# Optimization experiments

Measured on AMD Instinct MI355X. Metric: run time of the kernel, lower is better.

Reference implementation:

```python
import jax, jax.numpy as jnp
import numpy as np

H = 128      # hidden_channels
C = 5        # input_channels
B = 2048     # batch
G = 10       # grid size


def _conv(x, w, b, pad):
    # x: [B,Cin,H,W], w: [Cout,Cin,kh,kw]
    y = jax.lax.conv_general_dilated(
        x, w, window_strides=(1, 1), padding=[(pad, pad), (pad, pad)],
        dimension_numbers=('NCHW', 'OIHW', 'NCHW'))
    return y + b[None, :, None, None]


def setup_inputs() -> dict:
    key = jax.random.key(0)
    ks = jax.random.split(key, 16)
    s = 0.05  # weight init scale
    inp = {
        'x': jax.random.uniform(ks[0], (B, C, G, G), dtype=jnp.float32),
        'w_p1': jax.random.normal(ks[1], (H, C, 3, 3), jnp.float32) * s,
        'b_p1': jnp.zeros((H,), jnp.float32),
        'w_p2': jax.random.normal(ks[2], (H, H, 3, 3), jnp.float32) * s,
        'b_p2': jnp.zeros((H,), jnp.float32),
        'w_p3': jax.random.normal(ks[3], (H, H, 1, 1), jnp.float32) * s,
        'b_p3': jnp.zeros((H,), jnp.float32),
        'w_u1': jax.random.normal(ks[4], (H, H, 1, 1), jnp.float32) * s,
        'b_u1': jnp.zeros((H,), jnp.float32),
        'w_u2': jax.random.normal(ks[5], (H, H, 1, 1), jnp.float32) * s,
        'b_u2': jnp.zeros((H,), jnp.float32),
        'w_u3': jax.random.normal(ks[6], (H, H, 1, 1), jnp.float32) * s,
        'b_u3': jnp.zeros((H,), jnp.float32),
        'w_u4': jax.random.normal(ks[7], (C, H, 1, 1), jnp.float32) * s,
        'b_u4': jnp.zeros((C,), jnp.float32),
        'steps': 50,
    }
    return inp


def reference(x, w_p1, b_p1, w_p2, b_p2, w_p3, b_p3,
              w_u1, b_u1, w_u2, b_u2, w_u3, b_u3, w_u4, b_u4, steps):
    relu = jax.nn.relu
    steps_f = jnp.float32(steps)

    def step_fn(x, step):
        dx = relu(_conv(x, w_p1, b_p1, 1))
        dx = relu(_conv(dx, w_p2, b_p2, 1))
        dx = relu(_conv(dx, w_p3, b_p3, 0))
        dx = relu(_conv(dx, w_u1, b_u1, 0))
        dx = relu(_conv(dx, w_u2, b_u2, 0))
        dx = relu(_conv(dx, w_u3, b_u3, 0))
        dx = _conv(dx, w_u4, b_u4, 0)
        x = x + dx
        temperature = jnp.maximum(1.0 - step / steps_f, 0.5)
        x = jax.nn.softmax(x / temperature, axis=1)
        return x, x

    x_final, states = jax.lax.scan(step_fn, x, jnp.arange(steps, dtype=jnp.float32))
    # states: [steps, B, C, G, G] — stacked analogue of the python list
    return x_final, states
```

## Files before the change

kernel.cpp:

```cpp
#include <hip/hip_runtime.h>
#include <cstdint>
#include <cstddef>


#define NSAMPLES 2048
#define ZROW_BASE 28672
#define HA_OFF 0
#define HB_OFF 28928
#define A1_OFF HB_OFF
#define XS_OFF 57600
#define LDS_TOTAL 62976

typedef __attribute__((ext_vector_type(8))) short bf16x8;
typedef __attribute__((ext_vector_type(4))) float f32x4;
typedef __attribute__((ext_vector_type(2))) unsigned int u32x2;
typedef __attribute__((ext_vector_type(4))) unsigned int u32x4;

#define MFMA16(A,B,C) __builtin_amdgcn_mfma_f32_16x16x32_bf16((A),(B),(C),0,0,0)

__device__ __forceinline__ unsigned pk2(float a, float b) {
  unsigned r;
  asm("v_cvt_pk_bf16_f32 %0, %1, %2" : "=v"(r) : "v"(a), "v"(b));
  return r;
}
__device__ __forceinline__ unsigned pk2r(float a, float b) {
  return pk2(fmaxf(a, 0.f), fmaxf(b, 0.f));
}

__device__ __forceinline__ short f2bf(float f) {
  unsigned u = __float_as_uint(f);
  return (short)((u + 0x7FFFu + ((u >> 16) & 1u)) >> 16);
}

__global__ void prepack_kernel(const float* __restrict__ w, short* __restrict__ dst,
                               int mode, int ntc, int Kact, int Nact, int total) {
  int idx = blockIdx.x * 256 + threadIdx.x;
  if (idx >= total) return;
  int j = idx & 7, l = (idx >> 3) & 63, t = idx >> 9;
  int nt = t % ntc, kt = t / ntc;
  int kg = kt * 32 + (l >> 4) * 8 + j;
  int nn = nt * 16 + (l & 15);
  float v = 0.f;
  if (mode == 0) {
    if (kg < Kact && nn < Nact) v = w[nn * Kact + kg];
  } else if (mode == 1) {
    if (kg < 45) { int s = kg / 5, cin = kg - 5 * s; v = w[nn * 45 + cin * 9 + s]; }
  } else {
    int s = kt >> 2;
    int kk = (kt & 3) * 32 + (l >> 4) * 8 + j;
    v = w[nn * 1152 + kk * 9 + s];
  }
  dst[idx] = f2bf(v);
}

__device__ __forceinline__ void load_w4(bf16x8 (&W)[2][4], const short* __restrict__ p,
                                        int w, int l) {
#pragma unroll
  for (int mt = 0; mt < 2; ++mt)
#pragma unroll
    for (int kt = 0; kt < 4; ++kt)
      W[mt][kt] = *(const bf16x8*)&p[((kt * 8 + 2 * w + mt) * 64 + l) * 8];
}
__device__ __forceinline__ void load_b(f32x4 (&pb)[2], const float* __restrict__ bp,
                                       int w, int g) {
  pb[0] = *(const f32x4*)&bp[16 * (2 * w) + 4 * g];
  pb[1] = *(const f32x4*)&bp[16 * (2 * w + 1) + 4 * g];
}

__device__ __forceinline__ void chain_mfma(const bf16x8 (&W)[2][4], const f32x4 (&pb)[2],
                                           const char* lds, int rdb, f32x4 (&acc)[2][7]) {
#pragma unroll
  for (int qt = 0; qt < 7; ++qt) { acc[0][qt] = pb[0]; acc[1][qt] = pb[1]; }
#pragma unroll
  for (int kt = 0; kt < 4; ++kt) {
    const char* src = lds + (rdb ^ (kt << 6));
#pragma unroll
    for (int qt = 0; qt < 7; ++qt) {
      bf16x8 Bf = *(const bf16x8*)(src + qt * 4096);
      acc[0][qt] = MFMA16(W[0][kt], Bf, acc[0][qt]);
      acc[1][qt] = MFMA16(W[1][kt], Bf, acc[1][qt]);
    }
  }
}

__device__ __forceinline__ void store_h(const f32x4 (&acc)[2][7], char* lds,
                                        int wb0, int wb1) {
#pragma unroll
  for (int mt = 0; mt < 2; ++mt) {
    char* d = lds + (mt ? wb1 : wb0);
#pragma unroll
    for (int qt = 0; qt < 7; ++qt) {
      f32x4 v = acc[mt][qt];
      u32x2 wv = {pk2r(v.x, v.y), pk2r(v.z, v.w)};
      *(u32x2*)(d + qt * 4096) = wv;
    }
  }
}

__global__ __launch_bounds__(256, 2)
void nca_kernel(
    const float* __restrict__ x_in,
    const float* __restrict__ b1p, const float* __restrict__ b2p,
    const float* __restrict__ b3p, const float* __restrict__ b4p,
    const float* __restrict__ b5p, const float* __restrict__ b6p,
    const float* __restrict__ b7p,
    const short* __restrict__ W1, const short* __restrict__ W2,
    const short* __restrict__ W3,
    const short* __restrict__ W7,
    const int* __restrict__ steps_ptr, float* __restrict__ d_out) {
  __shared__ __align__(16) char lds[LDS_TOTAL];
  float* xs = (float*)(lds + XS_OFF);

  const int tid = threadIdx.x;
  const int sample = blockIdx.x;
  const int w = tid >> 6;
  const int l = tid & 63;
  const int n = l & 15;
  const int g = l >> 4;
  const int g16 = g << 4;
  const int swzc = (n & 7) << 4;
  const int steps = *steps_ptr;
  const float steps_f = (float)steps;
  const f32x4 fz = {0.f, 0.f, 0.f, 0.f};

  const int rdA = HA_OFF + n * 256 + (g16 ^ swzc);
  const int rdB = HB_OFF + n * 256 + (g16 ^ swzc);
  const int rd1 = A1_OFF + n * 128 + (g16 ^ swzc);
  const int wcol0 = ((64 * w) | (8 * g)) ^ swzc;
  const int wcol1 = ((64 * w + 32) | (8 * g)) ^ swzc;
  const int wbA0 = HA_OFF + n * 256 + wcol0, wbA1 = HA_OFF + n * 256 + wcol1;
  const int wbB0 = HB_OFF + n * 256 + wcol0, wbB1 = HB_OFF + n * 256 + wcol1;
  int zadj[7];
#pragma unroll
  for (int qt = 0; qt < 7; ++qt) zadj[qt] = HA_OFF + ZROW_BASE + g16 - 4096 * qt;

  int rc[7];
#pragma unroll
  for (int qt = 0; qt < 7; ++qt) {
    int p = 16 * qt + n;
    if (p < 100) { int r = p / 10; rc[qt] = r * 32 + (p - 10 * r); }
    else rc[qt] = 0x4000;
  }
  const int cA = tid / 100, pA = tid - 100 * cA;
  const int cB = (tid + 256) / 100, pB = tid + 256 - 100 * cB;
  const int offA = pA * 12 + cA, offB = pB * 12 + cB;

  if (tid < 64) *(unsigned*)(lds + HA_OFF + ZROW_BASE + tid * 4) = 0;
  xs[offA] = x_in[(size_t)sample * 500 + tid];
  if (tid < 244) xs[offB] = x_in[(size_t)sample * 500 + tid + 256];
  f32x4 b7v = fz;
  if (g == 0) b7v = *(const f32x4*)&b7p[0];
  else if (g == 1) b7v.x = b7p[4];
  __syncthreads();

  for (int step = 0; step < steps; ++step) {
    if (step > 0) {
      size_t sb = 1024000u + ((size_t)(step - 1) * NSAMPLES + sample) * 500u;
      __builtin_nontemporal_store(xs[offA], &d_out[sb + tid]);
      if (tid < 244) __builtin_nontemporal_store(xs[offB], &d_out[sb + tid + 256]);
    }
    if (tid < 112) {
      const int p = tid;
      const bool pv = p < 100;
      const int pc = pv ? p : 99;
      const int r = pc / 10, c0 = pc - 10 * r;
      float val[48];
#pragma unroll
      for (int s = 0; s < 9; ++s) {
        const int dr = s / 3 - 1, dc = s % 3 - 1;
        f32x4 xv = fz; float x4v = 0.f;
        if (pv && (unsigned)(r + dr) < 10u && (unsigned)(c0 + dc) < 10u) {
          const float* xr = &xs[(p + dr * 10 + dc) * 12];
          xv = *(const f32x4*)xr; x4v = xr[4];
        }
        val[5*s+0] = xv.x; val[5*s+1] = xv.y; val[5*s+2] = xv.z;
        val[5*s+3] = xv.w; val[5*s+4] = x4v;
      }
      val[45] = val[46] = val[47] = 0.f;
      unsigned wd[24];
#pragma unroll
      for (int i = 0; i < 24; ++i) wd[i] = pk2(val[2*i], val[2*i+1]);
      const int swzr = (p & 7) << 4;
      char* arow = lds + A1_OFF + p * 128;
#pragma unroll
      for (int j = 0; j < 6; ++j) {
        u32x4 wv = {wd[4*j], wd[4*j+1], wd[4*j+2], wd[4*j+3]};
        *(u32x4*)(arow + ((16 * j) ^ swzr)) = wv;
      }
      u32x4 z4 = {0, 0, 0, 0};
      *(u32x4*)(arow + (96 ^ swzr)) = z4;
      *(u32x4*)(arow + (112 ^ swzr)) = z4;
    }
    __syncthreads();

    {
      bf16x8 Wf[2][2];
#pragma unroll
      for (int mt = 0; mt < 2; ++mt)
#pragma unroll
        for (int kt = 0; kt < 2; ++kt)
          Wf[mt][kt] = *(const bf16x8*)&W1[((kt * 8 + 2 * w + mt) * 64 + l) * 8];
      f32x4 pb[2];
      load_b(pb, b1p, w, g);
      f32x4 acc[2][7];
#pragma unroll
      for (int qt = 0; qt < 7; ++qt) { acc[0][qt] = pb[0]; acc[1][qt] = pb[1]; }
#pragma unroll
      for (int kt = 0; kt < 2; ++kt) {
        const char* src = lds + (rd1 ^ (kt << 6));
#pragma unroll
        for (int qt = 0; qt < 7; ++qt) {
          bf16x8 Bf = *(const bf16x8*)(src + qt * 2048);
          acc[0][qt] = MFMA16(Wf[0][kt], Bf, acc[0][qt]);
          acc[1][qt] = MFMA16(Wf[1][kt], Bf, acc[1][qt]);
        }
      }
      store_h(acc, lds, wbA0, wbA1);
    }
    __syncthreads();

    {
      f32x4 acc[2][7];
      {
        f32x4 pb[2];
        load_b(pb, b2p, w, g);
#pragma unroll
        for (int qt = 0; qt < 7; ++qt) { acc[0][qt] = pb[0]; acc[1][qt] = pb[1]; }
      }
#pragma unroll 1
      for (int s = 0; s < 9; ++s) {
        const int s3 = s / 3;
        const int dr = s3 - 1, dc = s - 3 * s3 - 1;
        bf16x8 Wf[2][4];
        load_w4(Wf, W2 + s * 16384, w, l);
        const int ps = n + dr * 10 + dc;
        const int bs = HA_OFF + ps * 256 + (g16 ^ ((ps & 7) << 4));
#pragma unroll
        for (int qt = 0; qt < 7; ++qt) {
          bool ok = ((unsigned)((rc[qt] >> 5) + dr) < 10u) &&
                    ((unsigned)((rc[qt] & 31) + dc) < 10u);
          int va = ok ? bs : zadj[qt];
#pragma unroll
          for (int kt = 0; kt < 4; ++kt) {
            bf16x8 Bf = *(const bf16x8*)(lds + (va ^ (kt << 6)) + qt * 4096);
            acc[0][qt] = MFMA16(Wf[0][kt], Bf, acc[0][qt]);
            acc[1][qt] = MFMA16(Wf[1][kt], Bf, acc[1][qt]);
          }
        }
      }
      store_h(acc, lds, wbB0, wbB1);
    }
    __syncthreads();

#pragma unroll 1
    for (int li = 0; li < 4; ++li) {
      const float* bp = (li == 0) ? b3p : (li == 1) ? b4p : (li == 2) ? b5p : b6p;
      const int rdb = (li & 1) ? rdA : rdB;
      const int wb0 = (li & 1) ? wbB0 : wbA0;
      const int wb1 = (li & 1) ? wbB1 : wbA1;
      bf16x8 Wf[2][4];
      load_w4(Wf, W3 + li * 16384, w, l);
      f32x4 pb[2];
      load_b(pb, bp, w, g);
      f32x4 acc[2][7];
      chain_mfma(Wf, pb, lds, rdb, acc);
      store_h(acc, lds, wb0, wb1);
      __syncthreads();
    }

    {
      bf16x8 W7f[4];
#pragma unroll
      for (int kt = 0; kt < 4; ++kt)
        W7f[kt] = *(const bf16x8*)&W7[(kt * 64 + l) * 8];
      float invT = 1.f / fmaxf(1.f - (float)step / steps_f, 0.5f);
#pragma unroll
      for (int rep = 0; rep < 2; ++rep) {
        int qt = 2 * w + rep;
        if (qt < 7) {
          f32x4 a = b7v;
          int va7 = rdB + qt * 4096;
#pragma unroll
          for (int kt = 0; kt < 4; ++kt) {
            bf16x8 Bf = *(const bf16x8*)(lds + (va7 ^ (kt << 6)));
            a = MFMA16(W7f[kt], Bf, a);
          }
          float c4v = __shfl_xor(a.x, 16);
          int px = 16 * qt + n;
          if (g == 0 && px < 100) {
            float* xr = &xs[px * 12];
            f32x4 xo = *(f32x4*)xr; float x4 = xr[4];
            float v0 = (xo.x + a.x) * invT, v1 = (xo.y + a.y) * invT;
            float v2 = (xo.z + a.z) * invT, v3 = (xo.w + a.w) * invT;
            float v4 = (x4 + c4v) * invT;
            float m = fmaxf(fmaxf(fmaxf(v0, v1), fmaxf(v2, v3)), v4);
            float e0 = __expf(v0 - m), e1 = __expf(v1 - m), e2 = __expf(v2 - m);
            float e3 = __expf(v3 - m), e4 = __expf(v4 - m);
            float inv = 1.f / (e0 + e1 + e2 + e3 + e4);
            f32x4 pv = {e0 * inv, e1 * inv, e2 * inv, e3 * inv};
            *(f32x4*)xr = pv; xr[4] = e4 * inv;
          }
        }
      }
    }
    __syncthreads();
  }

  {
    size_t sb = 1024000u + ((size_t)(steps - 1) * NSAMPLES + sample) * 500u;
    size_t fb = (size_t)sample * 500u;
    float vA = xs[offA];
    __builtin_nontemporal_store(vA, &d_out[fb + tid]);
    __builtin_nontemporal_store(vA, &d_out[sb + tid]);
    if (tid < 244) {
      float vB = xs[offB];
      __builtin_nontemporal_store(vB, &d_out[fb + tid + 256]);
      __builtin_nontemporal_store(vB, &d_out[sb + tid + 256]);
    }
  }
}

extern "C" void kernel_launch(void* const* d_in, const int* in_sizes, int n_in,
                              void* d_out, int out_size, void* d_ws, size_t ws_size,
                              hipStream_t stream) {
  const float* x   = (const float*)d_in[0];
  const float* wp1 = (const float*)d_in[1];
  const float* bp1 = (const float*)d_in[2];
  const float* wp2 = (const float*)d_in[3];
  const float* bp2 = (const float*)d_in[4];
  const float* wp3 = (const float*)d_in[5];
  const float* bp3 = (const float*)d_in[6];
  const float* wu1 = (const float*)d_in[7];
  const float* bu1 = (const float*)d_in[8];
  const float* wu2 = (const float*)d_in[9];
  const float* bu2 = (const float*)d_in[10];
  const float* wu3 = (const float*)d_in[11];
  const float* bu3 = (const float*)d_in[12];
  const float* wu4 = (const float*)d_in[13];
  const float* bu4 = (const float*)d_in[14];
  const int* steps = (const int*)d_in[15];

  short* W1 = (short*)d_ws;
  short* W2 = W1 + 8192;
  short* W3 = W2 + 147456;
  short* W4 = W3 + 16384;
  short* W5 = W4 + 16384;
  short* W6 = W5 + 16384;
  short* W7 = W6 + 16384;

  prepack_kernel<<<(8192   + 255) / 256, 256, 0, stream>>>(wp1, W1, 1, 8, 45,   128, 8192);
  prepack_kernel<<<(147456 + 255) / 256, 256, 0, stream>>>(wp2, W2, 2, 8, 1152, 128, 147456);
  prepack_kernel<<<(16384  + 255) / 256, 256, 0, stream>>>(wp3, W3, 0, 8, 128,  128, 16384);
  prepack_kernel<<<(16384  + 255) / 256, 256, 0, stream>>>(wu1, W4, 0, 8, 128,  128, 16384);
  prepack_kernel<<<(16384  + 255) / 256, 256, 0, stream>>>(wu2, W5, 0, 8, 128,  128, 16384);
  prepack_kernel<<<(16384  + 255) / 256, 256, 0, stream>>>(wu3, W6, 0, 8, 128,  128, 16384);
  prepack_kernel<<<(2048   + 255) / 256, 256, 0, stream>>>(wu4, W7, 0, 1, 128,  5,   2048);

  nca_kernel<<<NSAMPLES, 256, 0, stream>>>(
      x, bp1, bp2, bp3, bu1, bu2, bu3, bu4,
      W1, W2, W3, W7, steps, (float*)d_out);
}
```

Before: 4.583 ms.

## Split MFMA work across waves by pixel tiles and drop 1x1-chain barriers

Each wave now owns two 16-pixel row tiles and computes all 128 output channels, in two 64-channel halves, instead of owning 32 channels across all seven pixel tiles. Because every wave reads and writes only its own pixel rows in the 1x1 chain, the per-layer __syncthreads there are removed. Weights are streamed from global memory per k-tile instead of being held in registers for the whole layer, and the W7 fragment load is hoisted out of the step loop. The cost is uneven load: wave 3 has only one tile while waves 0-2 have two, and weight reads through cache increase.

```diff
diff --git a/kernel.cpp b/kernel.cpp
--- a/kernel.cpp
+++ b/kernel.cpp
@@ -53,46 +53,21 @@
   dst[idx] = f2bf(v);
 }
 
-__device__ __forceinline__ void load_w4(bf16x8 (&W)[2][4], const short* __restrict__ p,
-                                        int w, int l) {
-#pragma unroll
-  for (int mt = 0; mt < 2; ++mt)
-#pragma unroll
-    for (int kt = 0; kt < 4; ++kt)
-      W[mt][kt] = *(const bf16x8*)&p[((kt * 8 + 2 * w + mt) * 64 + l) * 8];
-}
-__device__ __forceinline__ void load_b(f32x4 (&pb)[2], const float* __restrict__ bp,
-                                       int w, int g) {
-  pb[0] = *(const f32x4*)&bp[16 * (2 * w) + 4 * g];
-  pb[1] = *(const f32x4*)&bp[16 * (2 * w + 1) + 4 * g];
-}
-
-__device__ __forceinline__ void chain_mfma(const bf16x8 (&W)[2][4], const f32x4 (&pb)[2],
-                                           const char* lds, int rdb, f32x4 (&acc)[2][7]) {
-#pragma unroll
-  for (int qt = 0; qt < 7; ++qt) { acc[0][qt] = pb[0]; acc[1][qt] = pb[1]; }
-#pragma unroll
-  for (int kt = 0; kt < 4; ++kt) {
-    const char* src = lds + (rdb ^ (kt << 6));
-#pragma unroll
-    for (int qt = 0; qt < 7; ++qt) {
-      bf16x8 Bf = *(const bf16x8*)(src + qt * 4096);
-      acc[0][qt] = MFMA16(W[0][kt], Bf, acc[0][qt]);
-      acc[1][qt] = MFMA16(W[1][kt], Bf, acc[1][qt]);
-    }
-  }
-}
-
-__device__ __forceinline__ void store_h(const f32x4 (&acc)[2][7], char* lds,
-                                        int wb0, int wb1) {
-#pragma unroll
-  for (int mt = 0; mt < 2; ++mt) {
-    char* d = lds + (mt ? wb1 : wb0);
-#pragma unroll
-    for (int qt = 0; qt < 7; ++qt) {
-      f32x4 v = acc[mt][qt];
+__device__ __forceinline__ void store_pass(const f32x4 (&acc)[4][2], char* lds,
+                                           int dstoff, int row0, int h, int g8,
+                                           int swzc, int nq2) {
+#pragma unroll
+  for (int i = 0; i < 4; ++i) {
+    int wc = ((32 * (4 * h + i)) | g8) ^ swzc;
+    {
+      f32x4 v = acc[i][0];
       u32x2 wv = {pk2r(v.x, v.y), pk2r(v.z, v.w)};
-      *(u32x2*)(d + qt * 4096) = wv;
+      *(u32x2*)(lds + dstoff + row0 + wc) = wv;
+    }
+    if (nq2) {
+      f32x4 v = acc[i][1];
+      u32x2 wv = {pk2r(v.x, v.y), pk2r(v.z, v.w)};
+      *(u32x2*)(lds + dstoff + row0 + 4096 + wc) = wv;
     }
   }
 }
@@ -118,28 +93,27 @@
   const int n = l & 15;
   const int g = l >> 4;
   const int g16 = g << 4;
+  const int g8 = g << 3;
   const int swzc = (n & 7) << 4;
   const int steps = *steps_ptr;
   const float steps_f = (float)steps;
   const f32x4 fz = {0.f, 0.f, 0.f, 0.f};
 
+  const int qt0 = 2 * w;
+  const int nq2 = (w < 3);
+  const int row0 = (16 * qt0 + n) * 256;
+
   const int rdA = HA_OFF + n * 256 + (g16 ^ swzc);
   const int rdB = HB_OFF + n * 256 + (g16 ^ swzc);
   const int rd1 = A1_OFF + n * 128 + (g16 ^ swzc);
-  const int wcol0 = ((64 * w) | (8 * g)) ^ swzc;
-  const int wcol1 = ((64 * w + 32) | (8 * g)) ^ swzc;
-  const int wbA0 = HA_OFF + n * 256 + wcol0, wbA1 = HA_OFF + n * 256 + wcol1;
-  const int wbB0 = HB_OFF + n * 256 + wcol0, wbB1 = HB_OFF + n * 256 + wcol1;
-  int zadj[7];
-#pragma unroll
-  for (int qt = 0; qt < 7; ++qt) zadj[qt] = HA_OFF + ZROW_BASE + g16 - 4096 * qt;
-
-  int rc[7];
-#pragma unroll
-  for (int qt = 0; qt < 7; ++qt) {
-    int p = 16 * qt + n;
-    if (p < 100) { int r = p / 10; rc[qt] = r * 32 + (p - 10 * r); }
-    else rc[qt] = 0x4000;
+  const int za  = HA_OFF + ZROW_BASE + g16;
+
+  int rc0, rc1;
+  {
+    int p = 16 * qt0 + n;
+    if (p < 100) { int r = p / 10; rc0 = r * 32 + (p - 10 * r); } else rc0 = 0x4000;
+    p += 16;
+    if (p < 100) { int r = p / 10; rc1 = r * 32 + (p - 10 * r); } else rc1 = 0x4000;
   }
   const int cA = tid / 100, pA = tid - 100 * cA;
   const int cB = (tid + 256) / 100, pB = tid + 256 - 100 * cB;
@@ -148,6 +122,10 @@
   if (tid < 64) *(unsigned*)(lds + HA_OFF + ZROW_BASE + tid * 4) = 0;
   xs[offA] = x_in[(size_t)sample * 500 + tid];
   if (tid < 244) xs[offB] = x_in[(size_t)sample * 500 + tid + 256];
+  bf16x8 W7f[4];
+#pragma unroll
+  for (int kt = 0; kt < 4; ++kt)
+    W7f[kt] = *(const bf16x8*)&W7[(kt * 64 + l) * 8];
   f32x4 b7v = fz;
   if (g == 0) b7v = *(const f32x4*)&b7p[0];
   else if (g == 1) b7v.x = b7p[4];
@@ -193,86 +171,109 @@
     }
     __syncthreads();
 
-    {
-      bf16x8 Wf[2][2];
-#pragma unroll
-      for (int mt = 0; mt < 2; ++mt)
-#pragma unroll
-        for (int kt = 0; kt < 2; ++kt)
-          Wf[mt][kt] = *(const bf16x8*)&W1[((kt * 8 + 2 * w + mt) * 64 + l) * 8];
-      f32x4 pb[2];
-      load_b(pb, b1p, w, g);
-      f32x4 acc[2][7];
-#pragma unroll
-      for (int qt = 0; qt < 7; ++qt) { acc[0][qt] = pb[0]; acc[1][qt] = pb[1]; }
+#pragma unroll 1
+    for (int h = 0; h < 2; ++h) {
+      f32x4 acc[4][2];
+#pragma unroll
+      for (int i = 0; i < 4; ++i) {
+        f32x4 pb = *(const f32x4*)&b1p[(4*h + i) * 16 + 4 * g];
+        acc[i][0] = pb; acc[i][1] = pb;
+      }
 #pragma unroll
       for (int kt = 0; kt < 2; ++kt) {
-        const char* src = lds + (rd1 ^ (kt << 6));
-#pragma unroll
-        for (int qt = 0; qt < 7; ++qt) {
-          bf16x8 Bf = *(const bf16x8*)(src + qt * 2048);
-          acc[0][qt] = MFMA16(Wf[0][kt], Bf, acc[0][qt]);
-          acc[1][qt] = MFMA16(Wf[1][kt], Bf, acc[1][qt]);
-        }
-      }
-      store_h(acc, lds, wbA0, wbA1);
+        bf16x8 Wf[4];
+#pragma unroll
+        for (int i = 0; i < 4; ++i)
+          Wf[i] = *(const bf16x8*)&W1[((kt * 8 + 4*h + i) * 64 + l) * 8];
+        const char* s1 = lds + (rd1 ^ (kt << 6)) + qt0 * 2048;
+        bf16x8 Bf0 = *(const bf16x8*)s1;
+#pragma unroll
+        for (int i = 0; i < 4; ++i) acc[i][0] = MFMA16(Wf[i], Bf0, acc[i][0]);
+        if (nq2) {
+          bf16x8 Bf1 = *(const bf16x8*)(s1 + 2048);
+#pragma unroll
+          for (int i = 0; i < 4; ++i) acc[i][1] = MFMA16(Wf[i], Bf1, acc[i][1]);
+        }
+      }
+      store_pass(acc, lds, HA_OFF, row0, h, g8, swzc, nq2);
     }
     __syncthreads();
 
-    {
-      f32x4 acc[2][7];
-      {
-        f32x4 pb[2];
-        load_b(pb, b2p, w, g);
-#pragma unroll
-        for (int qt = 0; qt < 7; ++qt) { acc[0][qt] = pb[0]; acc[1][qt] = pb[1]; }
+#pragma unroll 1
+    for (int h = 0; h < 2; ++h) {
+      f32x4 acc[4][2];
+#pragma unroll
+      for (int i = 0; i < 4; ++i) {
+        f32x4 pb = *(const f32x4*)&b2p[(4*h + i) * 16 + 4 * g];
+        acc[i][0] = pb; acc[i][1] = pb;
       }
 #pragma unroll 1
       for (int s = 0; s < 9; ++s) {
         const int s3 = s / 3;
         const int dr = s3 - 1, dc = s - 3 * s3 - 1;
-        bf16x8 Wf[2][4];
-        load_w4(Wf, W2 + s * 16384, w, l);
         const int ps = n + dr * 10 + dc;
         const int bs = HA_OFF + ps * 256 + (g16 ^ ((ps & 7) << 4));
-#pragma unroll
-        for (int qt = 0; qt < 7; ++qt) {
-          bool ok = ((unsigned)((rc[qt] >> 5) + dr) < 10u) &&
-                    ((unsigned)((rc[qt] & 31) + dc) < 10u);
-          int va = ok ? bs : zadj[qt];
-#pragma unroll
-          for (int kt = 0; kt < 4; ++kt) {
-            bf16x8 Bf = *(const bf16x8*)(lds + (va ^ (kt << 6)) + qt * 4096);
-            acc[0][qt] = MFMA16(Wf[0][kt], Bf, acc[0][qt]);
-            acc[1][qt] = MFMA16(Wf[1][kt], Bf, acc[1][qt]);
+        const bool ok0 = ((unsigned)((rc0 >> 5) + dr) < 10u) &&
+                         ((unsigned)((rc0 & 31) + dc) < 10u);
+        const bool ok1 = ((unsigned)((rc1 >> 5) + dr) < 10u) &&
+                         ((unsigned)((rc1 & 31) + dc) < 10u);
+        const int va0 = ok0 ? (bs + qt0 * 4096) : za;
+        const int va1 = ok1 ? (bs + qt0 * 4096 + 4096) : za;
+#pragma unroll 2
+        for (int kt = 0; kt < 4; ++kt) {
+          bf16x8 Wf[4];
+#pragma unroll
+          for (int i = 0; i < 4; ++i)
+            Wf[i] = *(const bf16x8*)&W2[(((s * 4 + kt) * 8 + 4*h + i) * 64 + l) * 8];
+          bf16x8 Bf0 = *(const bf16x8*)(lds + (va0 ^ (kt << 6)));
+#pragma unroll
+          for (int i = 0; i < 4; ++i) acc[i][0] = MFMA16(Wf[i], Bf0, acc[i][0]);
+          if (nq2) {
+            bf16x8 Bf1 = *(const bf16x8*)(lds + (va1 ^ (kt << 6)));
+#pragma unroll
+            for (int i = 0; i < 4; ++i) acc[i][1] = MFMA16(Wf[i], Bf1, acc[i][1]);
           }
         }
       }
-      store_h(acc, lds, wbB0, wbB1);
+      store_pass(acc, lds, HB_OFF, row0, h, g8, swzc, nq2);
     }
     __syncthreads();
 
 #pragma unroll 1
     for (int li = 0; li < 4; ++li) {
+      const short* Wp = W3 + li * 16384;
       const float* bp = (li == 0) ? b3p : (li == 1) ? b4p : (li == 2) ? b5p : b6p;
       const int rdb = (li & 1) ? rdA : rdB;
-      const int wb0 = (li & 1) ? wbB0 : wbA0;
-      const int wb1 = (li & 1) ? wbB1 : wbA1;
-      bf16x8 Wf[2][4];
-      load_w4(Wf, W3 + li * 16384, w, l);
-      f32x4 pb[2];
-      load_b(pb, bp, w, g);
-      f32x4 acc[2][7];
-      chain_mfma(Wf, pb, lds, rdb, acc);
-      store_h(acc, lds, wb0, wb1);
-      __syncthreads();
+      const int dsto = (li & 1) ? HB_OFF : HA_OFF;
+#pragma unroll 1
+      for (int h = 0; h < 2; ++h) {
+        f32x4 acc[4][2];
+#pragma unroll
+        for (int i = 0; i < 4; ++i) {
+          f32x4 pb = *(const f32x4*)&bp[(4*h + i) * 16 + 4 * g];
+          acc[i][0] = pb; acc[i][1] = pb;
+        }
+#pragma unroll 2
+        for (int kt = 0; kt < 4; ++kt) {
+          bf16x8 Wf[4];
+#pragma unroll
+          for (int i = 0; i < 4; ++i)
+            Wf[i] = *(const bf16x8*)&Wp[((kt * 8 + 4*h + i) * 64 + l) * 8];
+          const char* sb = lds + (rdb ^ (kt << 6)) + qt0 * 4096;
+          bf16x8 Bf0 = *(const bf16x8*)sb;
+#pragma unroll
+          for (int i = 0; i < 4; ++i) acc[i][0] = MFMA16(Wf[i], Bf0, acc[i][0]);
+          if (nq2) {
+            bf16x8 Bf1 = *(const bf16x8*)(sb + 4096);
+#pragma unroll
+            for (int i = 0; i < 4; ++i) acc[i][1] = MFMA16(Wf[i], Bf1, acc[i][1]);
+          }
+        }
+        store_pass(acc, lds, dsto, row0, h, g8, swzc, nq2);
+      }
     }
 
     {
-      bf16x8 W7f[4];
-#pragma unroll
-      for (int kt = 0; kt < 4; ++kt)
-        W7f[kt] = *(const bf16x8*)&W7[(kt * 64 + l) * 8];
       float invT = 1.f / fmaxf(1.f - (float)step / steps_f, 0.5f);
 #pragma unroll
       for (int rep = 0; rep < 2; ++rep) {
```

After: 7.720 ms. +68.4%, slower.

## Split each sample's work across 8 waves with 512-thread blocks

Applied to the files above, without the earlier changes.

Doubles the block size from 256 to 512 threads. Each pair of waves now shares an output-channel slice and splits the 7 pixel tiles 4/3 between them, which halves per-thread accumulator registers and adds waves for latency hiding. The W7 fragment load is hoisted out of the step loop, and the final projection uses one tile per wave. The cost is twice the weight-fragment loads per block (each wave pair loads the same W slice) and more threads contending at each barrier. Launch bounds are raised to 512 threads with 4 blocks requested.

```diff
diff --git a/kernel.cpp b/kernel.cpp
--- a/kernel.cpp
+++ b/kernel.cpp
@@ -54,50 +54,40 @@
 }
 
 __device__ __forceinline__ void load_w4(bf16x8 (&W)[2][4], const short* __restrict__ p,
-                                        int w, int l) {
+                                        int wc, int l) {
 #pragma unroll
   for (int mt = 0; mt < 2; ++mt)
 #pragma unroll
     for (int kt = 0; kt < 4; ++kt)
-      W[mt][kt] = *(const bf16x8*)&p[((kt * 8 + 2 * w + mt) * 64 + l) * 8];
+      W[mt][kt] = *(const bf16x8*)&p[((kt * 8 + 2 * wc + mt) * 64 + l) * 8];
 }
 __device__ __forceinline__ void load_b(f32x4 (&pb)[2], const float* __restrict__ bp,
-                                       int w, int g) {
-  pb[0] = *(const f32x4*)&bp[16 * (2 * w) + 4 * g];
-  pb[1] = *(const f32x4*)&bp[16 * (2 * w + 1) + 4 * g];
-}
-
-__device__ __forceinline__ void chain_mfma(const bf16x8 (&W)[2][4], const f32x4 (&pb)[2],
-                                           const char* lds, int rdb, f32x4 (&acc)[2][7]) {
-#pragma unroll
-  for (int qt = 0; qt < 7; ++qt) { acc[0][qt] = pb[0]; acc[1][qt] = pb[1]; }
-#pragma unroll
-  for (int kt = 0; kt < 4; ++kt) {
-    const char* src = lds + (rdb ^ (kt << 6));
-#pragma unroll
-    for (int qt = 0; qt < 7; ++qt) {
-      bf16x8 Bf = *(const bf16x8*)(src + qt * 4096);
-      acc[0][qt] = MFMA16(W[0][kt], Bf, acc[0][qt]);
-      acc[1][qt] = MFMA16(W[1][kt], Bf, acc[1][qt]);
-    }
-  }
-}
-
-__device__ __forceinline__ void store_h(const f32x4 (&acc)[2][7], char* lds,
-                                        int wb0, int wb1) {
-#pragma unroll
-  for (int mt = 0; mt < 2; ++mt) {
-    char* d = lds + (mt ? wb1 : wb0);
-#pragma unroll
-    for (int qt = 0; qt < 7; ++qt) {
-      f32x4 v = acc[mt][qt];
-      u32x2 wv = {pk2r(v.x, v.y), pk2r(v.z, v.w)};
-      *(u32x2*)(d + qt * 4096) = wv;
-    }
-  }
-}
-
-__global__ __launch_bounds__(256, 2)
+                                       int wc, int g) {
+  pb[0] = *(const f32x4*)&bp[16 * (2 * wc) + 4 * g];
+  pb[1] = *(const f32x4*)&bp[16 * (2 * wc + 1) + 4 * g];
+}
+
+__device__ __forceinline__ void store_half(const f32x4 (&acc)[2][4], char* lds, int dsto,
+                                           int qtb, int n, int nq, int wcol0, int wcol1) {
+#pragma unroll
+  for (int qtl = 0; qtl < 4; ++qtl) {
+    if (qtl < nq) {
+      int row = (16 * (qtb + qtl) + n) * 256;
+      {
+        f32x4 v = acc[0][qtl];
+        u32x2 wv = {pk2r(v.x, v.y), pk2r(v.z, v.w)};
+        *(u32x2*)(lds + dsto + row + wcol0) = wv;
+      }
+      {
+        f32x4 v = acc[1][qtl];
+        u32x2 wv = {pk2r(v.x, v.y), pk2r(v.z, v.w)};
+        *(u32x2*)(lds + dsto + row + wcol1) = wv;
+      }
+    }
+  }
+}
+
+__global__ __launch_bounds__(512, 4)
 void nca_kernel(
     const float* __restrict__ x_in,
     const float* __restrict__ b1p, const float* __restrict__ b2p,
@@ -113,12 +103,16 @@
 
   const int tid = threadIdx.x;
   const int sample = blockIdx.x;
-  const int w = tid >> 6;
+  const int w  = tid >> 6;
+  const int wc = w >> 1;
+  const int wp = w & 1;
   const int l = tid & 63;
   const int n = l & 15;
   const int g = l >> 4;
   const int g16 = g << 4;
   const int swzc = (n & 7) << 4;
+  const int qtb = wp * 4;
+  const int nq  = wp ? 3 : 4;
   const int steps = *steps_ptr;
   const float steps_f = (float)steps;
   const f32x4 fz = {0.f, 0.f, 0.f, 0.f};
@@ -126,38 +120,36 @@
   const int rdA = HA_OFF + n * 256 + (g16 ^ swzc);
   const int rdB = HB_OFF + n * 256 + (g16 ^ swzc);
   const int rd1 = A1_OFF + n * 128 + (g16 ^ swzc);
-  const int wcol0 = ((64 * w) | (8 * g)) ^ swzc;
-  const int wcol1 = ((64 * w + 32) | (8 * g)) ^ swzc;
-  const int wbA0 = HA_OFF + n * 256 + wcol0, wbA1 = HA_OFF + n * 256 + wcol1;
-  const int wbB0 = HB_OFF + n * 256 + wcol0, wbB1 = HB_OFF + n * 256 + wcol1;
-  int zadj[7];
-#pragma unroll
-  for (int qt = 0; qt < 7; ++qt) zadj[qt] = HA_OFF + ZROW_BASE + g16 - 4096 * qt;
-
-  int rc[7];
-#pragma unroll
-  for (int qt = 0; qt < 7; ++qt) {
-    int p = 16 * qt + n;
-    if (p < 100) { int r = p / 10; rc[qt] = r * 32 + (p - 10 * r); }
-    else rc[qt] = 0x4000;
-  }
-  const int cA = tid / 100, pA = tid - 100 * cA;
-  const int cB = (tid + 256) / 100, pB = tid + 256 - 100 * cB;
-  const int offA = pA * 12 + cA, offB = pB * 12 + cB;
+  const int za  = HA_OFF + ZROW_BASE + g16;
+  const int wcol0 = ((32 * (2 * wc)) | (8 * g)) ^ swzc;
+  const int wcol1 = ((32 * (2 * wc + 1)) | (8 * g)) ^ swzc;
+
+  int rcq[4];
+#pragma unroll
+  for (int qtl = 0; qtl < 4; ++qtl) {
+    int p = 16 * (qtb + qtl) + n;
+    if (qtl < nq && p < 100) { int r = p / 10; rcq[qtl] = r * 32 + (p - 10 * r); }
+    else rcq[qtl] = 0x4000;
+  }
+  const int c5 = tid < 500 ? tid / 100 : 4;
+  const int p5 = tid - 100 * c5;
+  const int off5 = p5 * 12 + c5;
 
   if (tid < 64) *(unsigned*)(lds + HA_OFF + ZROW_BASE + tid * 4) = 0;
-  xs[offA] = x_in[(size_t)sample * 500 + tid];
-  if (tid < 244) xs[offB] = x_in[(size_t)sample * 500 + tid + 256];
+  if (tid < 500) xs[off5] = x_in[(size_t)sample * 500 + tid];
+  bf16x8 W7f[4];
+#pragma unroll
+  for (int kt = 0; kt < 4; ++kt)
+    W7f[kt] = *(const bf16x8*)&W7[(kt * 64 + l) * 8];
   f32x4 b7v = fz;
   if (g == 0) b7v = *(const f32x4*)&b7p[0];
   else if (g == 1) b7v.x = b7p[4];
   __syncthreads();
 
   for (int step = 0; step < steps; ++step) {
-    if (step > 0) {
+    if (step > 0 && tid < 500) {
       size_t sb = 1024000u + ((size_t)(step - 1) * NSAMPLES + sample) * 500u;
-      __builtin_nontemporal_store(xs[offA], &d_out[sb + tid]);
-      if (tid < 244) __builtin_nontemporal_store(xs[offB], &d_out[sb + tid + 256]);
+      __builtin_nontemporal_store(xs[off5], &d_out[sb + tid]);
     }
     if (tid < 112) {
       const int p = tid;
@@ -199,56 +191,60 @@
       for (int mt = 0; mt < 2; ++mt)
 #pragma unroll
         for (int kt = 0; kt < 2; ++kt)
-          Wf[mt][kt] = *(const bf16x8*)&W1[((kt * 8 + 2 * w + mt) * 64 + l) * 8];
+          Wf[mt][kt] = *(const bf16x8*)&W1[((kt * 8 + 2 * wc + mt) * 64 + l) * 8];
       f32x4 pb[2];
-      load_b(pb, b1p, w, g);
-      f32x4 acc[2][7];
-#pragma unroll
-      for (int qt = 0; qt < 7; ++qt) { acc[0][qt] = pb[0]; acc[1][qt] = pb[1]; }
+      load_b(pb, b1p, wc, g);
+      f32x4 acc[2][4];
+#pragma unroll
+      for (int qtl = 0; qtl < 4; ++qtl) { acc[0][qtl] = pb[0]; acc[1][qtl] = pb[1]; }
 #pragma unroll
       for (int kt = 0; kt < 2; ++kt) {
         const char* src = lds + (rd1 ^ (kt << 6));
 #pragma unroll
-        for (int qt = 0; qt < 7; ++qt) {
-          bf16x8 Bf = *(const bf16x8*)(src + qt * 2048);
-          acc[0][qt] = MFMA16(Wf[0][kt], Bf, acc[0][qt]);
-          acc[1][qt] = MFMA16(Wf[1][kt], Bf, acc[1][qt]);
-        }
-      }
-      store_h(acc, lds, wbA0, wbA1);
+        for (int qtl = 0; qtl < 4; ++qtl) {
+          if (qtl < nq) {
+            bf16x8 Bf = *(const bf16x8*)(src + (qtb + qtl) * 2048);
+            acc[0][qtl] = MFMA16(Wf[0][kt], Bf, acc[0][qtl]);
+            acc[1][qtl] = MFMA16(Wf[1][kt], Bf, acc[1][qtl]);
+          }
+        }
+      }
+      store_half(acc, lds, HA_OFF, qtb, n, nq, wcol0, wcol1);
     }
     __syncthreads();
 
     {
-      f32x4 acc[2][7];
+      f32x4 acc[2][4];
       {
         f32x4 pb[2];
-        load_b(pb, b2p, w, g);
-#pragma unroll
-        for (int qt = 0; qt < 7; ++qt) { acc[0][qt] = pb[0]; acc[1][qt] = pb[1]; }
+        load_b(pb, b2p, wc, g);
+#pragma unroll
+        for (int qtl = 0; qtl < 4; ++qtl) { acc[0][qtl] = pb[0]; acc[1][qtl] = pb[1]; }
       }
 #pragma unroll 1
       for (int s = 0; s < 9; ++s) {
         const int s3 = s / 3;
         const int dr = s3 - 1, dc = s - 3 * s3 - 1;
         bf16x8 Wf[2][4];
-        load_w4(Wf, W2 + s * 16384, w, l);
+        load_w4(Wf, W2 + s * 16384, wc, l);
         const int ps = n + dr * 10 + dc;
         const int bs = HA_OFF + ps * 256 + (g16 ^ ((ps & 7) << 4));
 #pragma unroll
-        for (int qt = 0; qt < 7; ++qt) {
-          bool ok = ((unsigned)((rc[qt] >> 5) + dr) < 10u) &&
-                    ((unsigned)((rc[qt] & 31) + dc) < 10u);
-          int va = ok ? bs : zadj[qt];
-#pragma unroll
-          for (int kt = 0; kt < 4; ++kt) {
-            bf16x8 Bf = *(const bf16x8*)(lds + (va ^ (kt << 6)) + qt * 4096);
-            acc[0][qt] = MFMA16(Wf[0][kt], Bf, acc[0][qt]);
-            acc[1][qt] = MFMA16(Wf[1][kt], Bf, acc[1][qt]);
+        for (int qtl = 0; qtl < 4; ++qtl) {
+          if (qtl < nq) {
+            bool ok = ((unsigned)((rcq[qtl] >> 5) + dr) < 10u) &&
+                      ((unsigned)((rcq[qtl] & 31) + dc) < 10u);
+            int va = ok ? (bs + (qtb + qtl) * 4096) : za;
+#pragma unroll
+            for (int kt = 0; kt < 4; ++kt) {
+              bf16x8 Bf = *(const bf16x8*)(lds + (va ^ (kt << 6)));
+              acc[0][qtl] = MFMA16(Wf[0][kt], Bf, acc[0][qtl]);
+              acc[1][qtl] = MFMA16(Wf[1][kt], Bf, acc[1][qtl]);
+            }
           }
         }
       }
-      store_h(acc, lds, wbB0, wbB1);
+      store_half(acc, lds, HB_OFF, qtb, n, nq, wcol0, wcol1);
     }
     __syncthreads();
 
@@ -256,67 +252,66 @@
     for (int li = 0; li < 4; ++li) {
       const float* bp = (li == 0) ? b3p : (li == 1) ? b4p : (li == 2) ? b5p : b6p;
       const int rdb = (li & 1) ? rdA : rdB;
-      const int wb0 = (li & 1) ? wbB0 : wbA0;
-      const int wb1 = (li & 1) ? wbB1 : wbA1;
+      const int dsto = (li & 1) ? HB_OFF : HA_OFF;
       bf16x8 Wf[2][4];
-      load_w4(Wf, W3 + li * 16384, w, l);
+      load_w4(Wf, W3 + li * 16384, wc, l);
       f32x4 pb[2];
-      load_b(pb, bp, w, g);
-      f32x4 acc[2][7];
-      chain_mfma(Wf, pb, lds, rdb, acc);
-      store_h(acc, lds, wb0, wb1);
+      load_b(pb, bp, wc, g);
+      f32x4 acc[2][4];
+#pragma unroll
+      for (int qtl = 0; qtl < 4; ++qtl) { acc[0][qtl] = pb[0]; acc[1][qtl] = pb[1]; }
+#pragma unroll
+      for (int kt = 0; kt < 4; ++kt) {
+        const char* src = lds + (rdb ^ (kt << 6));
+#pragma unroll
+        for (int qtl = 0; qtl < 4; ++qtl) {
+          if (qtl < nq) {
+            bf16x8 Bf = *(const bf16x8*)(src + (qtb + qtl) * 4096);
+            acc[0][qtl] = MFMA16(Wf[0][kt], Bf, acc[0][qtl]);
+            acc[1][qtl] = MFMA16(Wf[1][kt], Bf, acc[1][qtl]);
+          }
+        }
+      }
+      store_half(acc, lds, dsto, qtb, n, nq, wcol0, wcol1);
       __syncthreads();
     }
 
     {
-      bf16x8 W7f[4];
-#pragma unroll
-      for (int kt = 0; kt < 4; ++kt)
-        W7f[kt] = *(const bf16x8*)&W7[(kt * 64 + l) * 8];
       float invT = 1.f / fmaxf(1.f - (float)step / steps_f, 0.5f);
-#pragma unroll
-      for (int rep = 0; rep < 2; ++rep) {
-        int qt = 2 * w + rep;
-        if (qt < 7) {
-          f32x4 a = b7v;
-          int va7 = rdB + qt * 4096;
-#pragma unroll
-          for (int kt = 0; kt < 4; ++kt) {
-            bf16x8 Bf = *(const bf16x8*)(lds + (va7 ^ (kt << 6)));
-            a = MFMA16(W7f[kt], Bf, a);
-          }
-          float c4v = __shfl_xor(a.x, 16);
-          int px = 16 * qt + n;
-          if (g == 0 && px < 100) {
-            float* xr = &xs[px * 12];
-            f32x4 xo = *(f32x4*)xr; float x4 = xr[4];
-            float v0 = (xo.x + a.x) * invT, v1 = (xo.y + a.y) * invT;
-            float v2 = (xo.z + a.z) * invT, v3 = (xo.w + a.w) * invT;
-            float v4 = (x4 + c4v) * invT;
-            float m = fmaxf(fmaxf(fmaxf(v0, v1), fmaxf(v2, v3)), v4);
-            float e0 = __expf(v0 - m), e1 = __expf(v1 - m), e2 = __expf(v2 - m);
-            float e3 = __expf(v3 - m), e4 = __expf(v4 - m);
-            float inv = 1.f / (e0 + e1 + e2 + e3 + e4);
-            f32x4 pv = {e0 * inv, e1 * inv, e2 * inv, e3 * inv};
-            *(f32x4*)xr = pv; xr[4] = e4 * inv;
-          }
+      if (w < 7) {
+        f32x4 a = b7v;
+        int va7 = rdB + w * 4096;
+#pragma unroll
+        for (int kt = 0; kt < 4; ++kt) {
+          bf16x8 Bf = *(const bf16x8*)(lds + (va7 ^ (kt << 6)));
+          a = MFMA16(W7f[kt], Bf, a);
+        }
+        float c4v = __shfl_xor(a.x, 16);
+        int px = 16 * w + n;
+        if (g == 0 && px < 100) {
+          float* xr = &xs[px * 12];
+          f32x4 xo = *(f32x4*)xr; float x4 = xr[4];
+          float v0 = (xo.x + a.x) * invT, v1 = (xo.y + a.y) * invT;
+          float v2 = (xo.z + a.z) * invT, v3 = (xo.w + a.w) * invT;
+          float v4 = (x4 + c4v) * invT;
+          float m = fmaxf(fmaxf(fmaxf(v0, v1), fmaxf(v2, v3)), v4);
+          float e0 = __expf(v0 - m), e1 = __expf(v1 - m), e2 = __expf(v2 - m);
+          float e3 = __expf(v3 - m), e4 = __expf(v4 - m);
+          float inv = 1.f / (e0 + e1 + e2 + e3 + e4);
+          f32x4 pv = {e0 * inv, e1 * inv, e2 * inv, e3 * inv};
+          *(f32x4*)xr = pv; xr[4] = e4 * inv;
         }
       }
     }
     __syncthreads();
   }
 
-  {
+  if (tid < 500) {
     size_t sb = 1024000u + ((size_t)(steps - 1) * NSAMPLES + sample) * 500u;
     size_t fb = (size_t)sample * 500u;
-    float vA = xs[offA];
-    __builtin_nontemporal_store(vA, &d_out[fb + tid]);
-    __builtin_nontemporal_store(vA, &d_out[sb + tid]);
-    if (tid < 244) {
-      float vB = xs[offB];
-      __builtin_nontemporal_store(vB, &d_out[fb + tid + 256]);
-      __builtin_nontemporal_store(vB, &d_out[sb + tid + 256]);
-    }
+    float v = xs[off5];
+    __builtin_nontemporal_store(v, &d_out[fb + tid]);
+    __builtin_nontemporal_store(v, &d_out[sb + tid]);
   }
 }
 
@@ -356,7 +351,7 @@
   prepack_kernel<<<(16384  + 255) / 256, 256, 0, stream>>>(wu3, W6, 0, 8, 128,  128, 16384);
   prepack_kernel<<<(2048   + 255) / 256, 256, 0, stream>>>(wu4, W7, 0, 1, 128,  5,   2048);
 
-  nca_kernel<<<NSAMPLES, 256, 0, stream>>>(
+  nca_kernel<<<NSAMPLES, 512, 0, stream>>>(
       x, bp1, bp2, bp3, bu1, bu2, bu3, bu4,
       W1, W2, W3, W7, steps, (float*)d_out);
 }
```

Measured after the change: 5.502 ms. 1.2x slower.

## Shrink LDS footprint by compacting padded pixel rows and using planar state layout

Applied to the files above, without the earlier changes.

Hidden-activation buffers now hold only 100 real pixel rows instead of 112. The seventh pixel tile reads a shared zero row for lanes past pixel 100 and sends their writes to a dummy slot. The state buffer moves from pixel-major with stride 12 to channel-planar, which removes the offset tables and gives a simple indexed load and store. Total LDS drops from about 62 KB to about 53 KB, which may allow more blocks per CU, at the cost of extra per-lane address selects and scalar LDS reads in the im2col and softmax stages.

```diff
diff --git a/kernel.cpp b/kernel.cpp
--- a/kernel.cpp
+++ b/kernel.cpp
@@ -4,12 +4,13 @@
 
 
 #define NSAMPLES 2048
-#define ZROW_BASE 28672
 #define HA_OFF 0
-#define HB_OFF 28928
+#define HB_OFF 25600
 #define A1_OFF HB_OFF
-#define XS_OFF 57600
-#define LDS_TOTAL 62976
+#define ZB_OFF 51200
+#define DP_OFF 51456
+#define XS_OFF 51712
+#define LDS_TOTAL 53712
 
 typedef __attribute__((ext_vector_type(8))) short bf16x8;
 typedef __attribute__((ext_vector_type(4))) float f32x4;
@@ -67,33 +68,44 @@
   pb[1] = *(const f32x4*)&bp[16 * (2 * w + 1) + 4 * g];
 }
 
-__device__ __forceinline__ void chain_mfma(const bf16x8 (&W)[2][4], const f32x4 (&pb)[2],
-                                           const char* lds, int rdb, f32x4 (&acc)[2][7]) {
+__device__ __forceinline__ void chain7(const bf16x8 (&W)[2][4], const f32x4 (&pb)[2],
+                                       const char* lds, int rdb, int rb6,
+                                       f32x4 (&acc)[2][7]) {
 #pragma unroll
   for (int qt = 0; qt < 7; ++qt) { acc[0][qt] = pb[0]; acc[1][qt] = pb[1]; }
 #pragma unroll
   for (int kt = 0; kt < 4; ++kt) {
     const char* src = lds + (rdb ^ (kt << 6));
 #pragma unroll
-    for (int qt = 0; qt < 7; ++qt) {
+    for (int qt = 0; qt < 6; ++qt) {
       bf16x8 Bf = *(const bf16x8*)(src + qt * 4096);
       acc[0][qt] = MFMA16(W[0][kt], Bf, acc[0][qt]);
       acc[1][qt] = MFMA16(W[1][kt], Bf, acc[1][qt]);
     }
-  }
-}
-
-__device__ __forceinline__ void store_h(const f32x4 (&acc)[2][7], char* lds,
-                                        int wb0, int wb1) {
-#pragma unroll
-  for (int mt = 0; mt < 2; ++mt) {
-    char* d = lds + (mt ? wb1 : wb0);
-#pragma unroll
-    for (int qt = 0; qt < 7; ++qt) {
-      f32x4 v = acc[mt][qt];
-      u32x2 wv = {pk2r(v.x, v.y), pk2r(v.z, v.w)};
-      *(u32x2*)(d + qt * 4096) = wv;
-    }
+    bf16x8 B6 = *(const bf16x8*)(lds + (rb6 ^ (kt << 6)));
+    acc[0][6] = MFMA16(W[0][kt], B6, acc[0][6]);
+    acc[1][6] = MFMA16(W[1][kt], B6, acc[1][6]);
+  }
+}
+
+__device__ __forceinline__ void store7(const f32x4 (&acc)[2][7], char* lds,
+                                       int wb0, int wb1, int w6b0, int w6b1) {
+#pragma unroll
+  for (int qt = 0; qt < 6; ++qt) {
+    f32x4 v0 = acc[0][qt];
+    u32x2 a = {pk2r(v0.x, v0.y), pk2r(v0.z, v0.w)};
+    *(u32x2*)(lds + wb0 + qt * 4096) = a;
+    f32x4 v1 = acc[1][qt];
+    u32x2 b = {pk2r(v1.x, v1.y), pk2r(v1.z, v1.w)};
+    *(u32x2*)(lds + wb1 + qt * 4096) = b;
+  }
+  {
+    f32x4 v0 = acc[0][6];
+    u32x2 a = {pk2r(v0.x, v0.y), pk2r(v0.z, v0.w)};
+    *(u32x2*)(lds + w6b0) = a;
+    f32x4 v1 = acc[1][6];
+    u32x2 b = {pk2r(v1.x, v1.y), pk2r(v1.z, v1.w)};
+    *(u32x2*)(lds + w6b1) = b;
   }
 }
 
@@ -109,7 +121,7 @@
     const short* __restrict__ W7,
     const int* __restrict__ steps_ptr, float* __restrict__ d_out) {
   __shared__ __align__(16) char lds[LDS_TOTAL];
-  float* xs = (float*)(lds + XS_OFF);
+  float* xsf = (float*)(lds + XS_OFF);
 
   const int tid = threadIdx.x;
   const int sample = blockIdx.x;
@@ -126,13 +138,19 @@
   const int rdA = HA_OFF + n * 256 + (g16 ^ swzc);
   const int rdB = HB_OFF + n * 256 + (g16 ^ swzc);
   const int rd1 = A1_OFF + n * 128 + (g16 ^ swzc);
+  const int zb  = ZB_OFF + g16;
+  const bool v6 = (n < 4);
+  const int rb6A = v6 ? (rdA + 24576) : zb;
+  const int rb6B = v6 ? (rdB + 24576) : zb;
+  const int rb61 = v6 ? (rd1 + 12288) : zb;
   const int wcol0 = ((64 * w) | (8 * g)) ^ swzc;
   const int wcol1 = ((64 * w + 32) | (8 * g)) ^ swzc;
   const int wbA0 = HA_OFF + n * 256 + wcol0, wbA1 = HA_OFF + n * 256 + wcol1;
   const int wbB0 = HB_OFF + n * 256 + wcol0, wbB1 = HB_OFF + n * 256 + wcol1;
-  int zadj[7];
-#pragma unroll
-  for (int qt = 0; qt < 7; ++qt) zadj[qt] = HA_OFF + ZROW_BASE + g16 - 4096 * qt;
+  const int w6A0 = v6 ? (wbA0 + 24576) : DP_OFF;
+  const int w6A1 = v6 ? (wbA1 + 24576) : DP_OFF;
+  const int w6B0 = v6 ? (wbB0 + 24576) : DP_OFF;
+  const int w6B1 = v6 ? (wbB1 + 24576) : DP_OFF;
 
   int rc[7];
 #pragma unroll
@@ -141,13 +159,10 @@
     if (p < 100) { int r = p / 10; rc[qt] = r * 32 + (p - 10 * r); }
     else rc[qt] = 0x4000;
   }
-  const int cA = tid / 100, pA = tid - 100 * cA;
-  const int cB = (tid + 256) / 100, pB = tid + 256 - 100 * cB;
-  const int offA = pA * 12 + cA, offB = pB * 12 + cB;
-
-  if (tid < 64) *(unsigned*)(lds + HA_OFF + ZROW_BASE + tid * 4) = 0;
-  xs[offA] = x_in[(size_t)sample * 500 + tid];
-  if (tid < 244) xs[offB] = x_in[(size_t)sample * 500 + tid + 256];
+
+  if (tid < 64) *(unsigned*)(lds + ZB_OFF + tid * 4) = 0;
+  xsf[tid < 500 ? tid : 500 - 1] = x_in[(size_t)sample * 500 + (tid < 500 ? tid : 499)];
+  if (tid < 244) xsf[tid + 256] = x_in[(size_t)sample * 500 + tid + 256];
   f32x4 b7v = fz;
   if (g == 0) b7v = *(const f32x4*)&b7p[0];
   else if (g == 1) b7v.x = b7p[4];
@@ -156,25 +171,24 @@
   for (int step = 0; step < steps; ++step) {
     if (step > 0) {
       size_t sb = 1024000u + ((size_t)(step - 1) * NSAMPLES + sample) * 500u;
-      __builtin_nontemporal_store(xs[offA], &d_out[sb + tid]);
-      if (tid < 244) __builtin_nontemporal_store(xs[offB], &d_out[sb + tid + 256]);
-    }
-    if (tid < 112) {
+      if (tid < 500) __builtin_nontemporal_store(xsf[tid], &d_out[sb + tid]);
+      if (tid < 244) __builtin_nontemporal_store(xsf[tid + 256], &d_out[sb + tid + 256]);
+    }
+    if (tid < 100) {
       const int p = tid;
-      const bool pv = p < 100;
-      const int pc = pv ? p : 99;
-      const int r = pc / 10, c0 = pc - 10 * r;
+      const int r = p / 10, c0 = p - 10 * r;
       float val[48];
 #pragma unroll
       for (int s = 0; s < 9; ++s) {
         const int dr = s / 3 - 1, dc = s % 3 - 1;
-        f32x4 xv = fz; float x4v = 0.f;
-        if (pv && (unsigned)(r + dr) < 10u && (unsigned)(c0 + dc) < 10u) {
-          const float* xr = &xs[(p + dr * 10 + dc) * 12];
-          xv = *(const f32x4*)xr; x4v = xr[4];
-        }
-        val[5*s+0] = xv.x; val[5*s+1] = xv.y; val[5*s+2] = xv.z;
-        val[5*s+3] = xv.w; val[5*s+4] = x4v;
+        bool okp = ((unsigned)(r + dr) < 10u) && ((unsigned)(c0 + dc) < 10u);
+        int p2 = okp ? (p + dr * 10 + dc) : p;
+        float m = okp ? 1.f : 0.f;
+        val[5*s+0] = xsf[p2] * m;
+        val[5*s+1] = xsf[100 + p2] * m;
+        val[5*s+2] = xsf[200 + p2] * m;
+        val[5*s+3] = xsf[300 + p2] * m;
+        val[5*s+4] = xsf[400 + p2] * m;
       }
       val[45] = val[46] = val[47] = 0.f;
       unsigned wd[24];
@@ -209,13 +223,16 @@
       for (int kt = 0; kt < 2; ++kt) {
         const char* src = lds + (rd1 ^ (kt << 6));
 #pragma unroll
-        for (int qt = 0; qt < 7; ++qt) {
+        for (int qt = 0; qt < 6; ++qt) {
           bf16x8 Bf = *(const bf16x8*)(src + qt * 2048);
           acc[0][qt] = MFMA16(Wf[0][kt], Bf, acc[0][qt]);
           acc[1][qt] = MFMA16(Wf[1][kt], Bf, acc[1][qt]);
         }
-      }
-      store_h(acc, lds, wbA0, wbA1);
+        bf16x8 B6 = *(const bf16x8*)(lds + (rb61 ^ (kt << 6)));
+        acc[0][6] = MFMA16(Wf[0][kt], B6, acc[0][6]);
+        acc[1][6] = MFMA16(Wf[1][kt], B6, acc[1][6]);
+      }
+      store7(acc, lds, wbA0, wbA1, w6A0, w6A1);
     }
     __syncthreads();
 
@@ -239,16 +256,16 @@
         for (int qt = 0; qt < 7; ++qt) {
           bool ok = ((unsigned)((rc[qt] >> 5) + dr) < 10u) &&
                     ((unsigned)((rc[qt] & 31) + dc) < 10u);
-          int va = ok ? bs : zadj[qt];
+          int va = ok ? (bs + qt * 4096) : zb;
 #pragma unroll
           for (int kt = 0; kt < 4; ++kt) {
-            bf16x8 Bf = *(const bf16x8*)(lds + (va ^ (kt << 6)) + qt * 4096);
+            bf16x8 Bf = *(const bf16x8*)(lds + (va ^ (kt << 6)));
             acc[0][qt] = MFMA16(Wf[0][kt], Bf, acc[0][qt]);
             acc[1][qt] = MFMA16(Wf[1][kt], Bf, acc[1][qt]);
           }
         }
       }
-      store_h(acc, lds, wbB0, wbB1);
+      store7(acc, lds, wbB0, wbB1, w6B0, w6B1);
     }
     __syncthreads();
 
@@ -256,15 +273,18 @@
     for (int li = 0; li < 4; ++li) {
       const float* bp = (li == 0) ? b3p : (li == 1) ? b4p : (li == 2) ? b5p : b6p;
       const int rdb = (li & 1) ? rdA : rdB;
+      const int rb6 = (li & 1) ? rb6A : rb6B;
       const int wb0 = (li & 1) ? wbB0 : wbA0;
       const int wb1 = (li & 1) ? wbB1 : wbA1;
+      const int w60 = (li & 1) ? w6B0 : w6A0;
+      const int w61 = (li & 1) ? w6B1 : w6A1;
       bf16x8 Wf[2][4];
       load_w4(Wf, W3 + li * 16384, w, l);
       f32x4 pb[2];
       load_b(pb, bp, w, g);
       f32x4 acc[2][7];
-      chain_mfma(Wf, pb, lds, rdb, acc);
-      store_h(acc, lds, wb0, wb1);
+      chain7(Wf, pb, lds, rdb, rb6, acc);
+      store7(acc, lds, wb0, wb1, w60, w61);
       __syncthreads();
     }
 
@@ -279,7 +299,7 @@
         int qt = 2 * w + rep;
         if (qt < 7) {
           f32x4 a = b7v;
-          int va7 = rdB + qt * 4096;
+          int va7 = (qt < 6 || v6) ? (rdB + qt * 4096) : zb;
 #pragma unroll
           for (int kt = 0; kt < 4; ++kt) {
             bf16x8 Bf = *(const bf16x8*)(lds + (va7 ^ (kt << 6)));
@@ -288,17 +308,17 @@
           float c4v = __shfl_xor(a.x, 16);
           int px = 16 * qt + n;
           if (g == 0 && px < 100) {
-            float* xr = &xs[px * 12];
-            f32x4 xo = *(f32x4*)xr; float x4 = xr[4];
-            float v0 = (xo.x + a.x) * invT, v1 = (xo.y + a.y) * invT;
-            float v2 = (xo.z + a.z) * invT, v3 = (xo.w + a.w) * invT;
+            float* xc = xsf + px;
+            float x0 = xc[0], x1 = xc[100], x2 = xc[200], x3 = xc[300], x4 = xc[400];
+            float v0 = (x0 + a.x) * invT, v1 = (x1 + a.y) * invT;
+            float v2 = (x2 + a.z) * invT, v3 = (x3 + a.w) * invT;
             float v4 = (x4 + c4v) * invT;
             float m = fmaxf(fmaxf(fmaxf(v0, v1), fmaxf(v2, v3)), v4);
             float e0 = __expf(v0 - m), e1 = __expf(v1 - m), e2 = __expf(v2 - m);
             float e3 = __expf(v3 - m), e4 = __expf(v4 - m);
             float inv = 1.f / (e0 + e1 + e2 + e3 + e4);
-            f32x4 pv = {e0 * inv, e1 * inv, e2 * inv, e3 * inv};
-            *(f32x4*)xr = pv; xr[4] = e4 * inv;
+            xc[0] = e0 * inv; xc[100] = e1 * inv; xc[200] = e2 * inv;
+            xc[300] = e3 * inv; xc[400] = e4 * inv;
           }
         }
       }
@@ -309,13 +329,15 @@
   {
     size_t sb = 1024000u + ((size_t)(steps - 1) * NSAMPLES + sample) * 500u;
     size_t fb = (size_t)sample * 500u;
-    float vA = xs[offA];
-    __builtin_nontemporal_store(vA, &d_out[fb + tid]);
-    __builtin_nontemporal_store(vA, &d_out[sb + tid]);
+    if (tid < 500) {
+      float v = xsf[tid];
+      __builtin_nontemporal_store(v, &d_out[fb + tid]);
+      __builtin_nontemporal_store(v, &d_out[sb + tid]);
+    }
     if (tid < 244) {
-      float vB = xs[offB];
-      __builtin_nontemporal_store(vB, &d_out[fb + tid + 256]);
-      __builtin_nontemporal_store(vB, &d_out[sb + tid + 256]);
+      float v = xsf[tid + 256];
+      __builtin_nontemporal_store(v, &d_out[fb + tid + 256]);
+      __builtin_nontemporal_store(v, &d_out[sb + tid + 256]);
     }
   }
 }
```

New measurement: 4.595 ms. No clear change (+0.3%).
